# Kernel tuning notes

Measured on AMD Instinct MI355X. Metric: run time of the kernel, lower is better.

## Reference

```python
import jax, jax.numpy as jnp
import numpy as np

DIM, DIN, NST, RK, K, BATCH, H, W = 64, 128, 16, 4, 4, 1, 128, 128


def conv2d(x, w, b=None, pad=0, groups=1):
    y = jax.lax.conv_general_dilated(x, w, (1, 1), [(pad, pad), (pad, pad)],
                                     dimension_numbers=('NCHW', 'OIHW', 'NCHW'),
                                     feature_group_count=groups)
    return y if b is None else y + b[None, :, None, None]


def layer_norm(x, g, b, eps=1e-5):
    mu = x.mean(-1, keepdims=True)
    var = x.var(-1, keepdims=True)
    return (x - mu) * jax.lax.rsqrt(var + eps) * g + b


def selective_scan(u, delta, A, Bs, Cs, D):
    # u, delta: (B,K,Din,L); A: (K,Din,N); Bs,Cs: (B,K,N,L); D: (K,Din)
    uT = jnp.moveaxis(u, -1, 0)
    dT = jnp.moveaxis(delta, -1, 0)
    BT = jnp.moveaxis(Bs, -1, 0)
    CT = jnp.moveaxis(Cs, -1, 0)
    h0 = jnp.zeros(u.shape[:3] + (A.shape[-1],), u.dtype)

    def step(h, inp):
        u_t, d_t, B_t, C_t = inp
        h = h * jnp.exp(d_t[..., None] * A) + (d_t * u_t)[..., None] * B_t[:, :, None, :]
        return h, jnp.einsum('bkdn,bkn->bkd', h, C_t)

    _, ys = jax.lax.scan(step, h0, (uT, dT, BT, CT))
    return jnp.moveaxis(ys, 0, -1) + u * D[None, :, :, None]


def ss2d(x, in_proj_w, conv_dw_w, conv_dw_b, x_proj_w, dt_w, dt_b, A_logs, Ds, on_g, on_b, out_w):
    # x: (B,H,W,C) -- VMamba-style SS2D with 4 scan directions
    Bb, Hh, Ww, C = x.shape
    L = Hh * Ww
    xz = jnp.einsum('bhwc,ec->bhwe', x, in_proj_w)
    xa, z = jnp.split(xz, 2, axis=-1)
    xa = jax.nn.silu(conv2d(xa.transpose(0, 3, 1, 2), conv_dw_w, conv_dw_b, pad=1, groups=DIN))
    x0 = xa.reshape(Bb, DIN, L)                          # row-major scan
    x1 = xa.transpose(0, 1, 3, 2).reshape(Bb, DIN, L)    # column-major scan
    xs = jnp.stack([x0, x1, jnp.flip(x0, -1), jnp.flip(x1, -1)], axis=1)  # (B,4,Din,L)
    x_dbl = jnp.einsum('bkdl,kcd->bkcl', xs, x_proj_w)
    dts, Bs, Cs = x_dbl[:, :, :RK], x_dbl[:, :, RK:RK + NST], x_dbl[:, :, RK + NST:]
    delta = jax.nn.softplus(jnp.einsum('bkrl,kdr->bkdl', dts, dt_w) + dt_b[None, :, :, None])
    ys = selective_scan(xs, delta, -jnp.exp(A_logs), Bs, Cs, Ds)  # (B,4,Din,L)

    def unwh(t):
        return t.reshape(Bb, DIN, Ww, Hh).transpose(0, 1, 3, 2).reshape(Bb, DIN, L)

    y = ys[:, 0] + jnp.flip(ys[:, 2], -1) + unwh(ys[:, 1]) + unwh(jnp.flip(ys[:, 3], -1))
    y = layer_norm(y.transpose(0, 2, 1).reshape(Bb, Hh, Ww, DIN), on_g, on_b)
    return jnp.einsum('bhwd,cd->bhwc', y * jax.nn.silu(z), out_w)


def setup_inputs():
    key = jax.random.key(0)
    ks = jax.random.split(key, 24)
    n = lambda k, s, sc=0.05: jax.random.normal(k, s, jnp.float32) * sc
    return dict(
        x=n(ks[0], (BATCH, DIM, H, W), 1.0),
        conv1_w=n(ks[1], (DIM, DIM, 3, 3)), conv1_b=n(ks[2], (DIM,)),
        conv2_w=n(ks[3], (DIM, DIM, 5, 5)), conv2_b=n(ks[4], (DIM,)),
        dw1a_w=n(ks[5], (2 * DIM, 2, 3, 3)), dw1a_b=n(ks[6], (2 * DIM,)),
        dw1b_w=n(ks[7], (DIM, 2 * DIM, 1, 1)), dw1b_b=n(ks[8], (DIM,)),
        dw2a_w=n(ks[9], (DIM, 1, 3, 3)), dw2a_b=n(ks[10], (DIM,)),
        dw2b_w=n(ks[11], (DIM, DIM, 1, 1)), dw2b_b=n(ks[12], (DIM,)),
        ln_g=jnp.ones((DIM,), jnp.float32), ln_b=jnp.zeros((DIM,), jnp.float32),
        in_proj_w=n(ks[13], (2 * DIN, DIM)),
        conv_dw_w=n(ks[14], (DIN, 1, 3, 3)), conv_dw_b=n(ks[15], (DIN,)),
        x_proj_w=n(ks[16], (K, RK + 2 * NST, DIN)),
        dt_w=n(ks[17], (K, DIN, RK)), dt_b=jnp.full((K, DIN), 0.01, jnp.float32),
        A_logs=jnp.tile(jnp.log(jnp.arange(1, NST + 1, dtype=jnp.float32)), (K, DIN, 1)),
        Ds=jnp.ones((K, DIN), jnp.float32),
        on_g=jnp.ones((DIN,), jnp.float32), on_b=jnp.zeros((DIN,), jnp.float32),
        out_w=n(ks[18], (DIM, DIN)),
    )


def reference(x, conv1_w, conv1_b, conv2_w, conv2_b, dw1a_w, dw1a_b, dw1b_w, dw1b_b,
              dw2a_w, dw2a_b, dw2b_w, dw2b_b, ln_g, ln_b, in_proj_w, conv_dw_w, conv_dw_b,
              x_proj_w, dt_w, dt_b, A_logs, Ds, on_g, on_b, out_w):
    res = x
    y = jax.nn.relu(jnp.concatenate([conv2d(x, conv1_w, conv1_b, pad=1),
                                     conv2d(x, conv2_w, conv2_b, pad=2)], axis=1))
    y = jax.nn.relu(conv2d(conv2d(y, dw1a_w, dw1a_b, pad=1, groups=DIM), dw1b_w, dw1b_b))
    # F.layer_norm over (C,H,W), no affine
    mu = y.mean((1, 2, 3), keepdims=True)
    var = y.var((1, 2, 3), keepdims=True)
    y = (y - mu) * jax.lax.rsqrt(var + 1e-5)
    # SS2D block: pre-LN + SS2D + residual, in NHWC
    yp = y.transpose(0, 2, 3, 1)
    yp = yp + ss2d(layer_norm(yp, ln_g, ln_b), in_proj_w, conv_dw_w, conv_dw_b,
                   x_proj_w, dt_w, dt_b, A_logs, Ds, on_g, on_b, out_w)
    y = yp.transpose(0, 3, 1, 2)
    y = jax.nn.relu(conv2d(conv2d(y, dw2a_w, dw2a_b, pad=1, groups=DIM), dw2b_w, dw2b_b))
    return y + res
```

## Files before the change

### kernel.cpp

```cpp
#include <hip/hip_runtime.h>

#define L 16384
#define NCH 128
#define CT  128
#define PH 132
#define PW 136

__device__ __forceinline__ float softplusf(float x){
  return (x > 20.f) ? x : log1pf(__expf(x));
}
__device__ __forceinline__ float siluf(float x){
  return x / (1.f + __expf(-x));
}
__device__ __forceinline__ float wave_sum(float v){
  #pragma unroll
  for (int o = 32; o; o >>= 1) v += __shfl_xor(v, o);
  return v;
}

__global__ __launch_bounds__(256) void k_prep(
    const float* __restrict__ w1, const float* __restrict__ w2,
    const float* __restrict__ ipw,
    float* __restrict__ wT1, float* __restrict__ wT2, float* __restrict__ ipwT)
{
  int g = blockIdx.x * 256 + threadIdx.x;
  if (g < 36864){
    int ci = g / 576, rem = g % 576, co = rem / 9, tap = rem % 9;
    wT1[g] = w1[(co*64 + ci)*9 + tap];
  } else if (g < 36864 + 102400){
    int g2 = g - 36864;
    int ci = g2 / 1600, rem = g2 % 1600, co = rem / 25, tap = rem % 25;
    wT2[g2] = w2[(co*64 + ci)*25 + tap];
  } else if (g < 36864 + 102400 + 16384){
    int g3 = g - 139264;
    int e = g3 & 255, c = g3 >> 8;
    ipwT[g3] = ipw[e*64 + c];
  }
}

__global__ __launch_bounds__(256) void k_pad(
    const float* __restrict__ x, float* __restrict__ xpad)
{
  int g = blockIdx.x * 256 + threadIdx.x;
  int ci = g / (PH*PW);
  int r  = (g / PW) % PH;
  int c  = g % PW;
  float v = 0.f;
  int ur = r - 2, uc = c - 2;
  if ((unsigned)ur < 128u && (unsigned)uc < 128u)
    v = x[ci*L + ur*128 + uc];
  xpad[g] = v;
}

template<int KS>
__global__ __launch_bounds__(256) void k_convD(
    const float* __restrict__ xpad, const float* __restrict__ wT,
    float* __restrict__ part)
{
  constexpr int P = KS/2, NT = KS*KS;
  const int tid = threadIdx.x;
  const int col = tid & 127;
  const int rh  = tid >> 7;
  const int b   = blockIdx.x;
  const int cg  = b & 15;
  const int rq  = (b >> 4) & 31;
  const int s   = b >> 9;
  const int r0  = rq*4 + rh*2;
  const int co0 = cg*4;
  float acc[2][4];
  #pragma unroll
  for (int q = 0; q < 2; ++q)
    #pragma unroll
    for (int a = 0; a < 4; ++a) acc[q][a] = 0.f;

  const int ci0 = s*16;
  for (int ci = ci0; ci < ci0+16; ++ci){
    const float* xb = xpad + ci*(PH*PW) + (r0 - P + 2)*PW + (col - P + 2);
    const float* wp = wT + (ci*64 + co0)*NT;
    #pragma unroll
    for (int ir = 0; ir < KS+1; ++ir){
      float xrow[KS];
      #pragma unroll
      for (int kx = 0; kx < KS; ++kx) xrow[kx] = xb[ir*PW + kx];
      #pragma unroll
      for (int q = 0; q < 2; ++q){
        int ky = ir - q;
        if (ky >= 0 && ky < KS){
          #pragma unroll
          for (int kx = 0; kx < KS; ++kx){
            #pragma unroll
            for (int a = 0; a < 4; ++a)
              acc[q][a] = fmaf(xrow[kx], wp[a*NT + ky*KS + kx], acc[q][a]);
          }
        }
      }
    }
  }
  #pragma unroll
  for (int q = 0; q < 2; ++q){
    const int p = (r0+q)*128 + col;
    #pragma unroll
    for (int a = 0; a < 4; ++a)
      part[(s*64 + co0+a)*L + p] = acc[q][a];
  }
}

__global__ __launch_bounds__(256) void k_convred(
    const float* __restrict__ part1, const float* __restrict__ part2,
    const float* __restrict__ b1, const float* __restrict__ b2,
    float* __restrict__ y1)
{
  int g = blockIdx.x * 256 + threadIdx.x;
  int ch = g >> 14, p = g & (L-1);
  float v;
  if (ch < 64){
    v = b1[ch];
    #pragma unroll
    for (int s = 0; s < 4; ++s) v += part1[(s*64 + ch)*L + p];
  } else {
    int c = ch - 64;
    v = b2[c];
    #pragma unroll
    for (int s = 0; s < 4; ++s) v += part2[(s*64 + c)*L + p];
  }
  y1[ch*L + p] = fmaxf(v, 0.f);
}

__global__ __launch_bounds__(256) void k_dw1a(
    const float* __restrict__ y1, const float* __restrict__ w, const float* __restrict__ b,
    float* __restrict__ t1)
{
  int g = blockIdx.x * 256 + threadIdx.x;
  int p = g & (L-1);
  int o = g >> 14;
  int h = p >> 7, ww = p & 127;
  int grp = o >> 1;
  float acc = b[o];
  #pragma unroll
  for (int i = 0; i < 2; ++i){
    const float* xp = y1 + (grp*2 + i)*L;
    const float* wp = w + (o*2 + i)*9;
    #pragma unroll
    for (int ky = 0; ky < 3; ++ky){
      int hh = h + ky - 1;
      if ((unsigned)hh < 128u){
        #pragma unroll
        for (int kx = 0; kx < 3; ++kx){
          int wx = ww + kx - 1;
          if ((unsigned)wx < 128u)
            acc = fmaf(xp[hh*128 + wx], wp[ky*3+kx], acc);
        }
      }
    }
  }
  t1[o*L + p] = acc;
}

__global__ __launch_bounds__(256) void k_dw1b(
    const float* __restrict__ t1, const float* __restrict__ w, const float* __restrict__ b,
    float* __restrict__ y2, float* __restrict__ red)
{
  __shared__ float s[16][130];
  __shared__ float rs[4][2];
  int p0 = blockIdx.x * 16;
  for (int i = threadIdx.x; i < 2048; i += 256){
    int ci = i >> 4, dp = i & 15;
    s[dp][ci] = t1[ci*L + p0 + dp];
  }
  __syncthreads();
  int dp = threadIdx.x & 15, cg = threadIdx.x >> 4;
  float lsum = 0.f, lsq = 0.f;
  #pragma unroll
  for (int cc = 0; cc < 4; ++cc){
    int c = cg + cc*16;
    float acc = b[c];
    const float* wp = w + c*128;
    #pragma unroll 8
    for (int i = 0; i < 128; ++i) acc = fmaf(s[dp][i], wp[i], acc);
    acc = fmaxf(acc, 0.f);
    y2[c*L + p0 + dp] = acc;
    lsum += acc; lsq += acc*acc;
  }
  lsum = wave_sum(lsum); lsq = wave_sum(lsq);
  if ((threadIdx.x & 63) == 0){ rs[threadIdx.x>>6][0] = lsum; rs[threadIdx.x>>6][1] = lsq; }
  __syncthreads();
  if (threadIdx.x == 0){
    float a = rs[0][0]+rs[1][0]+rs[2][0]+rs[3][0];
    float q = rs[0][1]+rs[1][1]+rs[2][1]+rs[3][1];
    atomicAdd(&red[0], a);
    atomicAdd(&red[1], q);
  }
}

__global__ __launch_bounds__(256) void k_norm_inproj(
    const float* __restrict__ y2, const float* __restrict__ red,
    const float* __restrict__ ln_g, const float* __restrict__ ln_b,
    const float* __restrict__ ipwT,
    float* __restrict__ ynorm, float* __restrict__ xa_pre, float* __restrict__ sz)
{
  __shared__ float ws_s[16384];
  __shared__ float ls_s[64*33];
  __shared__ float mv_s[2][32];
  const int tid = threadIdx.x;
  const int p0 = blockIdx.x * 32;
  {
    const float4* src = (const float4*)ipwT;
    float4* dst = (float4*)ws_s;
    #pragma unroll
    for (int i = 0; i < 16; ++i) dst[tid + i*256] = src[tid + i*256];
  }
  const float invN = 1.f / 1048576.f;
  float mu = red[0] * invN;
  float var = red[1] * invN - mu*mu;
  float rsg = rsqrtf(var + 1e-5f);
  for (int i = tid; i < 2048; i += 256){
    int c = i >> 5, pix = i & 31;
    ls_s[c*33 + pix] = (y2[c*L + p0 + pix] - mu) * rsg;
  }
  __syncthreads();
  for (int i = tid; i < 2048; i += 256){
    int pix = i >> 6, c = i & 63;
    ynorm[(p0 + pix)*64 + c] = ls_s[c*33 + pix];
  }
  if (tid < 32){
    float s = 0.f, q = 0.f;
    #pragma unroll 8
    for (int c = 0; c < 64; ++c){
      float v = ls_s[c*33 + tid];
      s += v; q += v*v;
    }
    float m = s * (1.f/64.f);
    float va = q * (1.f/64.f) - m*m;
    mv_s[0][tid] = m;
    mv_s[1][tid] = rsqrtf(va + 1e-5f);
  }
  __syncthreads();
  for (int i = tid; i < 2048; i += 256){
    int c = i >> 5, pix = i & 31;
    float v = ls_s[c*33 + pix];
    ls_s[c*33 + pix] = (v - mv_s[0][pix]) * mv_s[1][pix] * ln_g[c] + ln_b[c];
  }
  __syncthreads();
  const int pix = tid & 31, eh = tid >> 5;
  float acc[32];
  #pragma unroll
  for (int j = 0; j < 32; ++j) acc[j] = 0.f;
  for (int c = 0; c < 64; ++c){
    float lnv = ls_s[c*33 + pix];
    const float4* w4 = (const float4*)(ws_s + c*256 + eh*32);
    #pragma unroll
    for (int j = 0; j < 8; ++j){
      float4 wq = w4[j];
      acc[j*4+0] = fmaf(lnv, wq.x, acc[j*4+0]);
      acc[j*4+1] = fmaf(lnv, wq.y, acc[j*4+1]);
      acc[j*4+2] = fmaf(lnv, wq.z, acc[j*4+2]);
      acc[j*4+3] = fmaf(lnv, wq.w, acc[j*4+3]);
    }
  }
  __syncthreads();
  float* szs = ws_s;
  const int p = p0 + pix;
  if (eh < 4){
    const int e0 = eh*32;
    #pragma unroll
    for (int j = 0; j < 32; ++j)
      xa_pre[(e0+j)*L + p] = acc[j];
  } else {
    const int j0 = (eh-4)*32;
    #pragma unroll
    for (int j = 0; j < 32; ++j)
      szs[pix*129 + j0 + j] = siluf(acc[j]);
  }
  __syncthreads();
  for (int i = tid; i < 32*128; i += 256){
    int pix2 = i >> 7, j = i & 127;
    sz[(p0 + pix2)*128 + j] = szs[pix2*129 + j];
  }
}

__global__ __launch_bounds__(256) void k_dwc(
    const float* __restrict__ xa, const float* __restrict__ w, const float* __restrict__ b,
    float* __restrict__ u)
{
  int g = blockIdx.x * 256 + threadIdx.x;
  int p = g & (L-1);
  int d = g >> 14;
  int h = p >> 7, ww = p & 127;
  const float* xp = xa + d*L;
  const float* wp = w + d*9;
  float acc = b[d];
  #pragma unroll
  for (int ky = 0; ky < 3; ++ky){
    int hh = h + ky - 1;
    if ((unsigned)hh < 128u){
      #pragma unroll
      for (int kx = 0; kx < 3; ++kx){
        int wx = ww + kx - 1;
        if ((unsigned)wx < 128u)
          acc = fmaf(xp[hh*128 + wx], wp[ky*3+kx], acc);
      }
    }
  }
  u[d*L + p] = siluf(acc);
}

template<int PASS>
__global__ __launch_bounds__(256) void k_proj(
    const float* __restrict__ u, const float* __restrict__ xw,
    const float* __restrict__ dtw, const float* __restrict__ dtb,
    float* __restrict__ delta_s, float* __restrict__ Bs, float* __restrict__ Cs,
    float* __restrict__ u_out)
{
  __shared__ float us[16][132];
  __shared__ float dts[16][2][4];
  int bb = blockIdx.x;
  int tid = threadIdx.x;
  for (int i = tid; i < 16*128; i += 256){
    int d = i >> 4, pix = i & 15;
    int idx = bb*16 + pix;
    int p;
    if (PASS == 0) p = idx;
    else           p = (idx & 127)*128 + (idx >> 7);
    us[pix][d] = u[d*L + p];
  }
  __syncthreads();
  for (int o = tid; o < 1152; o += 256){
    int pix = o / 72; int r = o % 72; int kk = r / 36; int c = r % 36;
    int k = (PASS == 0) ? kk*2 : kk*2 + 1;
    const float4* ur = (const float4*)(&us[pix][0]);
    const float4* wr = (const float4*)(xw + (k*36 + c)*128);
    float acc = 0.f;
    #pragma unroll
    for (int i = 0; i < 32; ++i){
      float4 a = ur[i], bw = wr[i];
      acc = fmaf(a.x, bw.x, acc); acc = fmaf(a.y, bw.y, acc);
      acc = fmaf(a.z, bw.z, acc); acc = fmaf(a.w, bw.w, acc);
    }
    int idx = bb*16 + pix;
    if (c < 4)        dts[pix][kk][c] = acc;
    else if (c < 20)  Bs[(k*L + idx)*16 + (c-4)]  = acc;
    else              Cs[(k*L + idx)*16 + (c-20)] = acc;
  }
  __syncthreads();
  int d = tid & 127, ph = tid >> 7;
  #pragma unroll
  for (int pp = 0; pp < 8; ++pp){
    int pix = pp*2 + ph;
    int idx = bb*16 + pix;
    #pragma unroll
    for (int kk = 0; kk < 2; ++kk){
      int k = (PASS == 0) ? kk*2 : kk*2 + 1;
      const float4 dw = *((const float4*)(dtw + (k*128 + d)*4));
      float acc = dtb[k*128 + d];
      acc = fmaf(dts[pix][kk][0], dw.x, acc);
      acc = fmaf(dts[pix][kk][1], dw.y, acc);
      acc = fmaf(dts[pix][kk][2], dw.z, acc);
      acc = fmaf(dts[pix][kk][3], dw.w, acc);
      delta_s[(k*L + idx)*128 + d] = softplusf(acc);
    }
    u_out[idx*128 + d] = us[pix][d];
  }
}

__global__ __launch_bounds__(256) void k_scan1(
    const float* __restrict__ delta_s, const float* __restrict__ u_row,
    const float* __restrict__ u_col, const float* __restrict__ Bs,
    const float* __restrict__ Alog, float* __restrict__ P, float* __restrict__ S)
{
  int blk = blockIdx.x;
  int k = blk >> 7, ch = blk & (NCH-1);
  int tid = threadIdx.x;
  int d = tid & 127, nh = tid >> 7;
  const float* u_s = (k & 1) ? u_col : u_row;
  float A[8], Pv[8], Sv[8];
  #pragma unroll
  for (int j = 0; j < 8; ++j){
    A[j] = -__expf(Alog[(k*128 + d)*16 + nh*8 + j]);
    Pv[j] = 1.f; Sv[j] = 0.f;
  }
  int base = ch*CT;
  for (int t = 0; t < CT; ++t){
    int tl = base + t;
    int pos = (k < 2) ? tl : (L-1 - tl);
    float dl = delta_s[(k*L + pos)*128 + d];
    float du = dl * u_s[pos*128 + d];
    const float* Br = Bs + (k*L + pos)*16 + nh*8;
    #pragma unroll
    for (int j = 0; j < 8; ++j){
      float a = __expf(dl * A[j]);
      Sv[j] = fmaf(Sv[j], a, du * Br[j]);
      Pv[j] *= a;
    }
  }
  #pragma unroll
  for (int j = 0; j < 8; ++j){
    int o = (blk*16 + nh*8 + j)*128 + d;
    P[o] = Pv[j]; S[o] = Sv[j];
  }
}

__global__ __launch_bounds__(256) void k_scan2(
    const float* __restrict__ P, const float* __restrict__ S, float* __restrict__ hst)
{
  int g = blockIdx.x * 256 + threadIdx.x;
  int d = g & 127, n = (g >> 7) & 15, k = g >> 11;
  float h = 0.f;
  for (int c = 0; c < NCH; ++c){
    int o = (((k*NCH + c)*16) + n)*128 + d;
    hst[o] = h;
    h = fmaf(P[o], h, S[o]);
  }
}

__global__ __launch_bounds__(256) void k_scan3(
    const float* __restrict__ delta_s, const float* __restrict__ u_row,
    const float* __restrict__ u_col, const float* __restrict__ Bs,
    const float* __restrict__ Cs, const float* __restrict__ Alog,
    const float* __restrict__ hst, float* __restrict__ ys)
{
  int blk = blockIdx.x;
  int k = blk >> 7, ch = blk & (NCH-1);
  int tid = threadIdx.x;
  int d = tid >> 1, nh = tid & 1;
  const float* u_s = (k & 1) ? u_col : u_row;
  float A[8], h[8];
  #pragma unroll
  for (int j = 0; j < 8; ++j){
    A[j] = -__expf(Alog[(k*128 + d)*16 + nh*8 + j]);
    h[j] = hst[(blk*16 + nh*8 + j)*128 + d];
  }
  int base = ch*CT;
  for (int t = 0; t < CT; ++t){
    int tl = base + t;
    int pos = (k < 2) ? tl : (L-1 - tl);
    float dl = delta_s[(k*L + pos)*128 + d];
    float du = dl * u_s[pos*128 + d];
    const float* Br = Bs + (k*L + pos)*16 + nh*8;
    const float* Cr = Cs + (k*L + pos)*16 + nh*8;
    float y = 0.f;
    #pragma unroll
    for (int j = 0; j < 8; ++j){
      float a = __expf(dl * A[j]);
      h[j] = fmaf(h[j], a, du * Br[j]);
      y = fmaf(h[j], Cr[j], y);
    }
    y += __shfl_xor(y, 1);
    if (nh == 0) ys[(k*L + pos)*128 + d] = y;
  }
}

__global__ __launch_bounds__(128) void k_combine(
    const float* __restrict__ ys, const float* __restrict__ u_row,
    const float* __restrict__ Ds, const float* __restrict__ on_g,
    const float* __restrict__ on_b, const float* __restrict__ sz,
    const float* __restrict__ out_w, const float* __restrict__ ynorm,
    float* __restrict__ yp2)
{
  __shared__ float gs[128];
  __shared__ float rbuf[2][2];
  int p = blockIdx.x;
  int d = threadIdx.x;
  int h = p >> 7, w = p & 127;
  int pT = w*128 + h;
  float y = ys[(0*L + p )*128 + d] + ys[(2*L + p )*128 + d]
          + ys[(1*L + pT)*128 + d] + ys[(3*L + pT)*128 + d];
  float sumD = Ds[d] + Ds[128 + d] + Ds[256 + d] + Ds[384 + d];
  y = fmaf(u_row[p*128 + d], sumD, y);
  float s = wave_sum(y);
  float sq = wave_sum(y*y);
  if ((d & 63) == 0){ rbuf[d>>6][0] = s; rbuf[d>>6][1] = sq; }
  __syncthreads();
  float ts = rbuf[0][0] + rbuf[1][0];
  float tq = rbuf[0][1] + rbuf[1][1];
  float m = ts * (1.f/128.f);
  float va = tq * (1.f/128.f) - m*m;
  float yn = (y - m) * rsqrtf(va + 1e-5f) * on_g[d] + on_b[d];
  gs[d] = yn * sz[p*128 + d];
  __syncthreads();
  if (d < 64){
    const float4* wr = (const float4*)(out_w + d*128);
    const float4* gr = (const float4*)gs;
    float acc = 0.f;
    #pragma unroll
    for (int i = 0; i < 32; ++i){
      float4 a = gr[i], bw = wr[i];
      acc = fmaf(a.x, bw.x, acc); acc = fmaf(a.y, bw.y, acc);
      acc = fmaf(a.z, bw.z, acc); acc = fmaf(a.w, bw.w, acc);
    }
    yp2[p*64 + d] = ynorm[p*64 + d] + acc;
  }
}

__global__ __launch_bounds__(256) void k_dw2a(
    const float* __restrict__ yp2, const float* __restrict__ w,
    const float* __restrict__ b, float* __restrict__ t2)
{
  int g = blockIdx.x * 256 + threadIdx.x;
  int c = g & 63;
  int p = g >> 6;
  int h = p >> 7, ww = p & 127;
  const float* wp = w + c*9;
  float acc = b[c];
  #pragma unroll
  for (int ky = 0; ky < 3; ++ky){
    int hh = h + ky - 1;
    if ((unsigned)hh < 128u){
      #pragma unroll
      for (int kx = 0; kx < 3; ++kx){
        int wx = ww + kx - 1;
        if ((unsigned)wx < 128u)
          acc = fmaf(yp2[(hh*128 + wx)*64 + c], wp[ky*3+kx], acc);
      }
    }
  }
  t2[p*64 + c] = acc;
}

__global__ __launch_bounds__(256) void k_dw2b(
    const float* __restrict__ t2, const float* __restrict__ w,
    const float* __restrict__ b, const float* __restrict__ x,
    float* __restrict__ out)
{
  __shared__ float s[16][65];
  int p0 = blockIdx.x * 16;
  for (int i = threadIdx.x; i < 1024; i += 256){
    int pix = i >> 6, c = i & 63;
    s[pix][c] = t2[(p0 + pix)*64 + c];
  }
  __syncthreads();
  int dp = threadIdx.x & 15, cg = threadIdx.x >> 4;
  #pragma unroll
  for (int cc = 0; cc < 4; ++cc){
    int c = cg + cc*16;
    float acc = b[c];
    const float* wp = w + c*64;
    #pragma unroll 8
    for (int i = 0; i < 64; ++i) acc = fmaf(s[dp][i], wp[i], acc);
    acc = fmaxf(acc, 0.f);
    int p = p0 + dp;
    out[c*L + p] = acc + x[c*L + p];
  }
}

extern "C" void kernel_launch(void* const* d_in, const int* in_sizes, int n_in,
                              void* d_out, int out_size, void* d_ws, size_t ws_size,
                              hipStream_t stream)
{
  const float* x       = (const float*)d_in[0];
  const float* conv1_w = (const float*)d_in[1];
  const float* conv1_b = (const float*)d_in[2];
  const float* conv2_w = (const float*)d_in[3];
  const float* conv2_b = (const float*)d_in[4];
  const float* dw1a_w  = (const float*)d_in[5];
  const float* dw1a_b  = (const float*)d_in[6];
  const float* dw1b_w  = (const float*)d_in[7];
  const float* dw1b_b  = (const float*)d_in[8];
  const float* dw2a_w  = (const float*)d_in[9];
  const float* dw2a_b  = (const float*)d_in[10];
  const float* dw2b_w  = (const float*)d_in[11];
  const float* dw2b_b  = (const float*)d_in[12];
  const float* ln_g    = (const float*)d_in[13];
  const float* ln_b    = (const float*)d_in[14];
  const float* ipw     = (const float*)d_in[15];
  const float* cdw_w   = (const float*)d_in[16];
  const float* cdw_b   = (const float*)d_in[17];
  const float* xw      = (const float*)d_in[18];
  const float* dtw     = (const float*)d_in[19];
  const float* dtb     = (const float*)d_in[20];
  const float* Alog    = (const float*)d_in[21];
  const float* DsArr   = (const float*)d_in[22];
  const float* on_g    = (const float*)d_in[23];
  const float* on_b    = (const float*)d_in[24];
  const float* out_w   = (const float*)d_in[25];
  float* out = (float*)d_out;

  char* ws = (char*)d_ws;
  const size_t MB = 1048576ull;
  float* y1      = (float*)(ws + 0*MB);
  float* t1      = (float*)(ws + 8*MB);
  float* y2      = (float*)(ws + 16*MB);
  float* xpad    = (float*)(ws + 20*MB);
  float* xa_pre  = (float*)(ws + 20*MB);
  float* wT1     = (float*)(ws + 28*MB);
  float* wT2     = (float*)(ws + 28*MB + 524288);
  float* ipwT    = (float*)(ws + 29*MB);
  float* red     = (float*)(ws + 30*MB);
  float* part1   = (float*)(ws + 32*MB);
  float* part2   = (float*)(ws + 48*MB);
  float* ysb     = (float*)(ws + 0*MB);
  float* delta_s = (float*)(ws + 32*MB);
  float* ynorm   = (float*)(ws + 64*MB);
  float* sz      = (float*)(ws + 68*MB);
  float* u       = (float*)(ws + 76*MB);
  float* u_row   = (float*)(ws + 84*MB);
  float* u_col   = (float*)(ws + 92*MB);
  float* Bsb     = (float*)(ws + 100*MB);
  float* Csb     = (float*)(ws + 104*MB);
  float* Pb      = (float*)(ws + 108*MB);
  float* Sb      = (float*)(ws + 112*MB);
  float* hst     = (float*)(ws + 116*MB);
  float* yp2     = (float*)(ws + 108*MB);
  float* t2      = (float*)(ws + 112*MB);

  hipMemsetAsync(red, 0, 2*sizeof(float), stream);

  k_prep    <<<608, 256, 0, stream>>>(conv1_w, conv2_w, ipw, wT1, wT2, ipwT);
  k_pad     <<<4488, 256, 0, stream>>>(x, xpad);
  k_convD<3><<<2048, 256, 0, stream>>>(xpad, wT1, part1);
  k_convD<5><<<2048, 256, 0, stream>>>(xpad, wT2, part2);
  k_convred <<<8192, 256, 0, stream>>>(part1, part2, conv1_b, conv2_b, y1);
  k_dw1a  <<<8192, 256, 0, stream>>>(y1, dw1a_w, dw1a_b, t1);
  k_dw1b  <<<1024, 256, 0, stream>>>(t1, dw1b_w, dw1b_b, y2, red);
  k_norm_inproj<<<512, 256, 0, stream>>>(y2, red, ln_g, ln_b, ipwT, ynorm, xa_pre, sz);
  k_dwc   <<<8192, 256, 0, stream>>>(xa_pre, cdw_w, cdw_b, u);
  k_proj<0><<<1024, 256, 0, stream>>>(u, xw, dtw, dtb, delta_s, Bsb, Csb, u_row);
  k_proj<1><<<1024, 256, 0, stream>>>(u, xw, dtw, dtb, delta_s, Bsb, Csb, u_col);
  k_scan1 <<<4*NCH, 256, 0, stream>>>(delta_s, u_row, u_col, Bsb, Alog, Pb, Sb);
  k_scan2 <<<32, 256, 0, stream>>>(Pb, Sb, hst);
  k_scan3 <<<4*NCH, 256, 0, stream>>>(delta_s, u_row, u_col, Bsb, Csb, Alog, hst, ysb);
  k_combine<<<16384, 128, 0, stream>>>(ysb, u_row, DsArr, on_g, on_b, sz, out_w, ynorm, yp2);
  k_dw2a  <<<4096, 256, 0, stream>>>(yp2, dw2a_w, dw2a_b, t2);
  k_dw2b  <<<1024, 256, 0, stream>>>(t2, dw2b_w, dw2b_b, x, out);
}
```

Before: 636.4 us.

## Pre-transpose u and rewrite x_proj to hold pixel rows in registers

A new tiled shared-memory transpose kernel writes a column-major copy of u, so the column-scan projection reads coalesced data instead of strided gathers. The projection kernel is restructured: each thread keeps one pixel's 128 channel values in registers and computes 18 of the 36 projection outputs for one direction, with weights read from global/scalar memory. Blocks now cover 64 pixels, giving 256 blocks per pass instead of 1024. The change adds an extra kernel launch and a 128-float register array per thread, which risks spills or low occupancy with so few blocks.

```diff
diff --git a/kernel.cpp b/kernel.cpp
--- a/kernel.cpp
+++ b/kernel.cpp
@@ -304,61 +304,88 @@
   u[d*L + p] = siluf(acc);
 }
 
+__global__ __launch_bounds__(256) void k_transp(
+    const float* __restrict__ u, float* __restrict__ uT)
+{
+  __shared__ float t[32][33];
+  int b = blockIdx.x;
+  int d = b >> 4;
+  int th = (b >> 2) & 3;
+  int tw = b & 3;
+  int lx = threadIdx.x & 31, ly = threadIdx.x >> 5;
+  const float* src = u + d*L;
+  #pragma unroll
+  for (int i = 0; i < 4; ++i)
+    t[ly + i*8][lx] = src[(th*32 + ly + i*8)*128 + tw*32 + lx];
+  __syncthreads();
+  float* dst = uT + d*L;
+  #pragma unroll
+  for (int i = 0; i < 4; ++i)
+    dst[(tw*32 + ly + i*8)*128 + th*32 + lx] = t[lx][ly + i*8];
+}
+
 template<int PASS>
-__global__ __launch_bounds__(256) void k_proj(
-    const float* __restrict__ u, const float* __restrict__ xw,
+__global__ __launch_bounds__(256) void k_projB(
+    const float* __restrict__ u_src, const float* __restrict__ xw,
     const float* __restrict__ dtw, const float* __restrict__ dtb,
     float* __restrict__ delta_s, float* __restrict__ Bs, float* __restrict__ Cs,
     float* __restrict__ u_out)
 {
-  __shared__ float us[16][132];
-  __shared__ float dts[16][2][4];
-  int bb = blockIdx.x;
-  int tid = threadIdx.x;
-  for (int i = tid; i < 16*128; i += 256){
-    int d = i >> 4, pix = i & 15;
-    int idx = bb*16 + pix;
-    int p;
-    if (PASS == 0) p = idx;
-    else           p = (idx & 127)*128 + (idx >> 7);
-    us[pix][d] = u[d*L + p];
-  }
-  __syncthreads();
-  for (int o = tid; o < 1152; o += 256){
-    int pix = o / 72; int r = o % 72; int kk = r / 36; int c = r % 36;
-    int k = (PASS == 0) ? kk*2 : kk*2 + 1;
-    const float4* ur = (const float4*)(&us[pix][0]);
-    const float4* wr = (const float4*)(xw + (k*36 + c)*128);
-    float acc = 0.f;
-    #pragma unroll
-    for (int i = 0; i < 32; ++i){
-      float4 a = ur[i], bw = wr[i];
-      acc = fmaf(a.x, bw.x, acc); acc = fmaf(a.y, bw.y, acc);
-      acc = fmaf(a.z, bw.z, acc); acc = fmaf(a.w, bw.w, acc);
-    }
-    int idx = bb*16 + pix;
-    if (c < 4)        dts[pix][kk][c] = acc;
-    else if (c < 20)  Bs[(k*L + idx)*16 + (c-4)]  = acc;
-    else              Cs[(k*L + idx)*16 + (c-20)] = acc;
-  }
-  __syncthreads();
-  int d = tid & 127, ph = tid >> 7;
-  #pragma unroll
-  for (int pp = 0; pp < 8; ++pp){
-    int pix = pp*2 + ph;
-    int idx = bb*16 + pix;
-    #pragma unroll
-    for (int kk = 0; kk < 2; ++kk){
-      int k = (PASS == 0) ? kk*2 : kk*2 + 1;
-      const float4 dw = *((const float4*)(dtw + (k*128 + d)*4));
-      float acc = dtb[k*128 + d];
-      acc = fmaf(dts[pix][kk][0], dw.x, acc);
-      acc = fmaf(dts[pix][kk][1], dw.y, acc);
-      acc = fmaf(dts[pix][kk][2], dw.z, acc);
-      acc = fmaf(dts[pix][kk][3], dw.w, acc);
-      delta_s[(k*L + idx)*128 + d] = softplusf(acc);
-    }
-    u_out[idx*128 + d] = us[pix][d];
+  __shared__ float dts_s[64][2][4];
+  const int tid = threadIdx.x;
+  const int pix = tid & 63;
+  const int grpu = __builtin_amdgcn_readfirstlane(tid >> 6);
+  const int half = grpu & 1, kk = grpu >> 1;
+  const int k = kk*2 + PASS;
+  const int idx0 = blockIdx.x * 64;
+  const int idx = idx0 + pix;
+
+  float urg[128];
+  #pragma unroll
+  for (int d = 0; d < 128; ++d){
+    urg[d] = u_src[d*L + idx];
+    if ((d >> 5) == grpu) u_out[idx*128 + d] = urg[d];
+  }
+
+  const float* wbase = xw + (k*36 + half*18)*128;
+  #pragma unroll
+  for (int j = 0; j < 18; ++j){
+    const float* wr = wbase + j*128;
+    float s0 = 0.f, s1 = 0.f, s2 = 0.f, s3 = 0.f;
+    #pragma unroll
+    for (int q = 0; q < 32; ++q){
+      s0 = fmaf(urg[q*4+0], wr[q*4+0], s0);
+      s1 = fmaf(urg[q*4+1], wr[q*4+1], s1);
+      s2 = fmaf(urg[q*4+2], wr[q*4+2], s2);
+      s3 = fmaf(urg[q*4+3], wr[q*4+3], s3);
+    }
+    float acc = (s0+s1)+(s2+s3);
+    if (half == 0){
+      if (j < 4) dts_s[pix][kk][j] = acc;
+      else       Bs[(k*L + idx)*16 + (j-4)] = acc;
+    } else {
+      if (j < 2) Bs[(k*L + idx)*16 + (14+j)] = acc;
+      else       Cs[(k*L + idx)*16 + (j-2)] = acc;
+    }
+  }
+  __syncthreads();
+
+  const int d = tid & 127, ph = tid >> 7;
+  #pragma unroll
+  for (int pp = 0; pp < 32; ++pp){
+    int px = pp*2 + ph;
+    int ix = idx0 + px;
+    #pragma unroll
+    for (int q = 0; q < 2; ++q){
+      int kq = q*2 + PASS;
+      const float4 dw = *((const float4*)(dtw + (kq*128 + d)*4));
+      float a = dtb[kq*128 + d];
+      a = fmaf(dts_s[px][q][0], dw.x, a);
+      a = fmaf(dts_s[px][q][1], dw.y, a);
+      a = fmaf(dts_s[px][q][2], dw.z, a);
+      a = fmaf(dts_s[px][q][3], dw.w, a);
+      delta_s[(kq*L + ix)*128 + d] = softplusf(a);
+    }
   }
 }
 
@@ -577,6 +604,7 @@
   char* ws = (char*)d_ws;
   const size_t MB = 1048576ull;
   float* y1      = (float*)(ws + 0*MB);
+  float* uT      = (float*)(ws + 0*MB);
   float* t1      = (float*)(ws + 8*MB);
   float* y2      = (float*)(ws + 16*MB);
   float* xpad    = (float*)(ws + 20*MB);
@@ -613,8 +641,9 @@
   k_dw1b  <<<1024, 256, 0, stream>>>(t1, dw1b_w, dw1b_b, y2, red);
   k_norm_inproj<<<512, 256, 0, stream>>>(y2, red, ln_g, ln_b, ipwT, ynorm, xa_pre, sz);
   k_dwc   <<<8192, 256, 0, stream>>>(xa_pre, cdw_w, cdw_b, u);
-  k_proj<0><<<1024, 256, 0, stream>>>(u, xw, dtw, dtb, delta_s, Bsb, Csb, u_row);
-  k_proj<1><<<1024, 256, 0, stream>>>(u, xw, dtw, dtb, delta_s, Bsb, Csb, u_col);
+  k_transp<<<2048, 256, 0, stream>>>(u, uT);
+  k_projB<0><<<256, 256, 0, stream>>>(u,  xw, dtw, dtb, delta_s, Bsb, Csb, u_row);
+  k_projB<1><<<256, 256, 0, stream>>>(uT, xw, dtw, dtb, delta_s, Bsb, Csb, u_col);
   k_scan1 <<<4*NCH, 256, 0, stream>>>(delta_s, u_row, u_col, Bsb, Alog, Pb, Sb);
   k_scan2 <<<32, 256, 0, stream>>>(Pb, Sb, hst);
   k_scan3 <<<4*NCH, 256, 0, stream>>>(delta_s, u_row, u_col, Bsb, Csb, Alog, hst, ysb);
```

After: 607.8 us. 1.05x faster.
